# Performance work log

Measured on AMD Instinct MI355X. Metric: run time of the kernel, lower is better.

Reference implementation:

```python
import jax, jax.numpy as jnp
import numpy as np

T, H, N = 4096, 32, 64

def setup_inputs() -> dict:
    key = jax.random.key(0)
    ks = jax.random.split(key, 7)
    r = jax.random.normal(ks[0], (T, H, N), dtype=jnp.float32)
    w = jax.random.uniform(ks[1], (T, H, N), dtype=jnp.float32)  # decay in (0,1)
    k = jax.random.normal(ks[2], (T, H, N), dtype=jnp.float32)
    v = jax.random.normal(ks[3], (T, H, N), dtype=jnp.float32)
    a = jax.random.normal(ks[4], (T, H, N), dtype=jnp.float32) * 0.1
    b = jax.random.normal(ks[5], (T, H, N), dtype=jnp.float32) * 0.1
    state = jax.random.normal(ks[6], (H, N, N), dtype=jnp.float32) * 0.1
    return {"r": r, "w": w, "k": k, "v": v, "a": a, "b": b, "state": state}


def reference(r, w, k, v, a, b, state):
    # RWKV7 WKV recurrence (BlinkDL v7 reference):
    #   S_t = S_{t-1} * diag(w_t) + S_{t-1} @ (a_t b_t^T) + v_t k_t^T
    #   y_t = S_t @ r_t
    # state: [H, N, N] with rows = value dim, cols = key dim.
    def step(S, inp):
        r_, w_, k_, v_, a_, b_ = inp  # each [H, N]
        ab = jnp.einsum('hi,hj->hij', a_, b_)           # [H, N, N]
        vk = jnp.einsum('hi,hj->hij', v_, k_)           # [H, N, N]
        S = S * w_[:, None, :] + jnp.einsum('hij,hjk->hik', S, ab) + vk
        y = jnp.einsum('hij,hj->hi', S, r_)             # [H, N]
        return S, y

    S_final, y = jax.lax.scan(step, state, (r, w, k, v, a, b))
    return y, S_final  # y: [T, H, N], S_final: [H, N, N]
```

## Files before the change

### kernel.cpp

```cpp
#include <hip/hip_runtime.h>
#include <hip/hip_bf16.h>


#define Tt 4096
#define Hh 32
#define Nn 64
#define Ll 64
#define Cc 64
#define HN (Hh * Nn)
#define NN (Nn * Nn)

__device__ __forceinline__ float ldf(const float* p) { return *p; }
__device__ __forceinline__ float ldf(const __hip_bfloat16* p) { return __bfloat162float(*p); }
__device__ __forceinline__ void stf(float* p, float v) { *p = v; }
__device__ __forceinline__ void stf(__hip_bfloat16* p, float v) { *p = __float2bfloat16(v); }

__device__ __forceinline__ float rl(float v, int j) {
    return __int_as_float(__builtin_amdgcn_readlane(__float_as_int(v), j));
}

__device__ __forceinline__ float bflo(unsigned u) { return __uint_as_float(u << 16); }
__device__ __forceinline__ float bfhi(unsigned u) { return __uint_as_float(u & 0xffff0000u); }

template <typename ST>
__global__ __launch_bounds__(128, 4)
void pass1_scan(const float* __restrict__ rr, const float* __restrict__ ww,
                const float* __restrict__ kk, const float* __restrict__ vv,
                const float* __restrict__ aa, const float* __restrict__ bb,
                float* __restrict__ ylocal,
                ST* __restrict__ rho, ST* __restrict__ Mt, ST* __restrict__ Pt)
{
    const int c    = blockIdx.x >> 5;
    const int h    = blockIdx.x & 31;
    const int tid  = threadIdx.x;
    const int lane = tid & 63;
    const int wv   = tid >> 6;
    const int j0   = __builtin_amdgcn_readfirstlane(wv << 5);

    __shared__ float2 ex1[2][2][64];
    __shared__ float  ex2[2][2][64];

    float SP[32];
    float SM[32];
    #pragma unroll
    for (int jj = 0; jj < 32; ++jj) {
        SP[jj] = 0.0f;
        SM[jj] = (j0 + jj == lane) ? 1.0f : 0.0f;
    }

    int base = (c * Ll * Hh + h) * Nn;
    const int lv = j0 + (lane & 31);
    float ca = aa[base + lv];
    float cw = ww[base + lv];
    float cb = bb[base + lv];
    float cr = rr[base + lv];
    float ck = kk[base + lv];
    float cv = vv[base + lane];

    float py = 0.f, pq = 0.f;

    for (int t = 0; t < Ll; ++t) {
        float p0 = 0.f, p1 = 0.f, m0 = 0.f, m1 = 0.f;
        #pragma unroll
        for (int jj = 0; jj < 32; jj += 2) {
            const float a0 = rl(ca, jj), a1 = rl(ca, jj + 1);
            p0 += SP[jj + 0] * a0;  m0 += SM[jj + 0] * a0;
            p1 += SP[jj + 1] * a1;  m1 += SM[jj + 1] * a1;
        }
        const float pP = p0 + p1, pM = m0 + m1;

        ex1[t & 1][wv][lane] = make_float2(pP, pM);
        if (t > 0) ex2[(t - 1) & 1][wv][lane] = (wv == 0) ? pq : py;
        __syncthreads();
        const float2 o = ex1[t & 1][wv ^ 1][lane];
        const float saP = pP + o.x;
        const float saM = pM + o.y;
        if (t > 0) {
            const int ob = base - HN + lane;
            if (wv == 0) ylocal[ob] = py + ex2[(t - 1) & 1][1][lane];
            else         stf(&rho[ob], pq + ex2[(t - 1) & 1][0][lane]);
        }

        float na = 0.f, nw = 0.f, nb = 0.f, nr = 0.f, nk = 0.f, nv = 0.f;
        if (t + 1 < Ll) {
            const int b2 = base + HN;
            na = aa[b2 + lv]; nw = ww[b2 + lv]; nb = bb[b2 + lv];
            nr = rr[b2 + lv]; nk = kk[b2 + lv]; nv = vv[b2 + lane];
        }

        float y0 = 0.f, y1 = 0.f, q0 = 0.f, q1 = 0.f;
        #pragma unroll
        for (int jj = 0; jj < 32; jj += 2) {
            const float w0 = rl(cw, jj), w1 = rl(cw, jj + 1);
            const float b0 = rl(cb, jj), b1 = rl(cb, jj + 1);
            const float k0 = rl(ck, jj), k1 = rl(ck, jj + 1);
            const float r0 = rl(cr, jj), r1 = rl(cr, jj + 1);
            SP[jj + 0] = SP[jj + 0] * w0 + saP * b0 + cv * k0;
            SP[jj + 1] = SP[jj + 1] * w1 + saP * b1 + cv * k1;
            SM[jj + 0] = SM[jj + 0] * w0 + saM * b0;
            SM[jj + 1] = SM[jj + 1] * w1 + saM * b1;
            y0 += SP[jj + 0] * r0;
            y1 += SP[jj + 1] * r1;
            q0 += SM[jj + 0] * r0;
            q1 += SM[jj + 1] * r1;
        }
        py = y0 + y1;
        pq = q0 + q1;

        base += HN;
        ca = na; cw = nw; cb = nb; cr = nr; ck = nk; cv = nv;
    }

    {
        ex2[(Ll - 1) & 1][wv][lane] = (wv == 0) ? pq : py;
        __syncthreads();
        const int ob = base - HN + lane;
        if (wv == 0) ylocal[ob] = py + ex2[(Ll - 1) & 1][1][lane];
        else         stf(&rho[ob], pq + ex2[(Ll - 1) & 1][0][lane]);
    }

    const size_t mb = ((size_t)(c * Hh) + h) * NN;
    #pragma unroll
    for (int jj = 0; jj < 32; ++jj) {
        stf(&Pt[mb + (size_t)(j0 + jj) * Nn + lane], SP[jj]);
        stf(&Mt[mb + (size_t)(j0 + jj) * Nn + lane], SM[jj]);
    }
}

#define LMS 68

template <typename ST>
__global__ __launch_bounds__(512, 2)
void pass2_chain(const ST* __restrict__ Mt, const ST* __restrict__ Pt,
                 const float* __restrict__ st0, ST* __restrict__ Sst,
                 float* __restrict__ sfin)
{
    const int bid = blockIdx.x;
    const int h   = bid & 31;
    const int g   = bid >> 5;
    const int tid = threadIdx.x;
    const int j   = tid & 63;
    const int wv  = tid >> 6;
    const int r   = g * 8 + wv;

    __shared__ float lm[2][Nn][LMS];

    float s = st0[(h * Nn + r) * Nn + j];

    {
        const size_t mb = (size_t)h * NN;
        if constexpr (sizeof(ST) == 2) {
            const uint4 u = *(const uint4*)&Mt[mb + (size_t)tid * 8];
            const int jj = tid >> 3, kc = (tid & 7) * 8;
            float4 f0, f1;
            f0.x = bflo(u.x); f0.y = bfhi(u.x); f0.z = bflo(u.y); f0.w = bfhi(u.y);
            f1.x = bflo(u.z); f1.y = bfhi(u.z); f1.z = bflo(u.w); f1.w = bfhi(u.w);
            *(float4*)&lm[0][jj][kc]     = f0;
            *(float4*)&lm[0][jj][kc + 4] = f1;
        } else {
            const float4 q0 = *(const float4*)&Mt[mb + (size_t)tid * 4];
            const float4 q1 = *(const float4*)&Mt[mb + 2048 + (size_t)tid * 4];
            const int jj = tid >> 4, kc = (tid * 4) & 63;
            *(float4*)&lm[0][jj][kc]      = q0;
            *(float4*)&lm[0][32 + jj][kc] = q1;
        }
    }
    float pp = ldf(&Pt[(size_t)h * NN + (size_t)j * Nn + r]);
    __syncthreads();

    for (int c = 0; c < Cc; ++c) {
        const int buf = c & 1;
        stf(&Sst[((size_t)(c * Hh) + h) * NN + (size_t)r * Nn + j], s);

        const bool pf = (c + 1 < Cc);
        const size_t nb = ((size_t)((c + 1) * Hh) + h) * NN;
        uint4 u = {0, 0, 0, 0};
        float4 q0 = {0, 0, 0, 0}, q1 = {0, 0, 0, 0};
        float ppn = 0.f;
        if (pf) {
            if constexpr (sizeof(ST) == 2) {
                u = *(const uint4*)&Mt[nb + (size_t)tid * 8];
            } else {
                q0 = *(const float4*)&Mt[nb + (size_t)tid * 4];
                q1 = *(const float4*)&Mt[nb + 2048 + (size_t)tid * 4];
            }
            ppn = ldf(&Pt[nb + (size_t)j * Nn + r]);
        }

        float a0 = pp, a1 = 0.f, a2 = 0.f, a3 = 0.f;
        #pragma unroll
        for (int m = 0; m < 16; ++m) {
            const float4 mv = *(const float4*)&lm[buf][j][4 * m];
            a0 += rl(s, 4 * m + 0) * mv.x;
            a1 += rl(s, 4 * m + 1) * mv.y;
            a2 += rl(s, 4 * m + 2) * mv.z;
            a3 += rl(s, 4 * m + 3) * mv.w;
        }

        if (pf) {
            if constexpr (sizeof(ST) == 2) {
                const int jj = tid >> 3, kc = (tid & 7) * 8;
                float4 f0, f1;
                f0.x = bflo(u.x); f0.y = bfhi(u.x); f0.z = bflo(u.y); f0.w = bfhi(u.y);
                f1.x = bflo(u.z); f1.y = bfhi(u.z); f1.z = bflo(u.w); f1.w = bfhi(u.w);
                *(float4*)&lm[buf ^ 1][jj][kc]     = f0;
                *(float4*)&lm[buf ^ 1][jj][kc + 4] = f1;
            } else {
                const int jj = tid >> 4, kc = (tid * 4) & 63;
                *(float4*)&lm[buf ^ 1][jj][kc]      = q0;
                *(float4*)&lm[buf ^ 1][32 + jj][kc] = q1;
            }
        }

        s = (a0 + a1) + (a2 + a3);
        pp = ppn;
        __syncthreads();
    }

    sfin[(h * Nn + r) * Nn + j] = s;
}

template <typename ST>
__global__ __launch_bounds__(256, 4)
void pass3_fix(const ST* __restrict__ rho, const ST* __restrict__ Sst,
               float* __restrict__ y)
{
    const int c    = blockIdx.x >> 5;
    const int h    = blockIdx.x & 31;
    const int tid  = threadIdx.x;
    const int lane = tid & 63;
    const int tq   = tid >> 6;

    __shared__ float ls[Nn][LMS];

    const size_t sb = ((size_t)(c * Hh) + h) * NN;
    if constexpr (sizeof(ST) == 2) {
        #pragma unroll
        for (int half = 0; half < 2; ++half) {
            const int e = half * 2048 + tid * 8;
            const uint4 u = *(const uint4*)&Sst[sb + e];
            const int jj = e >> 6, kc = e & 63;
            float4 f0, f1;
            f0.x = bflo(u.x); f0.y = bfhi(u.x); f0.z = bflo(u.y); f0.w = bfhi(u.y);
            f1.x = bflo(u.z); f1.y = bfhi(u.z); f1.z = bflo(u.w); f1.w = bfhi(u.w);
            *(float4*)&ls[jj][kc]     = f0;
            *(float4*)&ls[jj][kc + 4] = f1;
        }
    } else {
        #pragma unroll
        for (int qq = 0; qq < 4; ++qq) {
            const int e = qq * 1024 + tid * 4;
            const float4 v = *(const float4*)&Sst[sb + e];
            *(float4*)&ls[e >> 6][e & 63] = v;
        }
    }

    float rt[16];
    #pragma unroll
    for (int m = 0; m < 16; ++m)
        rt[m] = ldf(&rho[((size_t)(c * Ll + tq * 16 + m) * Hh + h) * Nn + lane]);

    __syncthreads();

    float Srow[Nn];
    #pragma unroll
    for (int m = 0; m < 16; ++m) {
        const float4 v = *(const float4*)&ls[lane][4 * m];
        Srow[4*m+0] = v.x; Srow[4*m+1] = v.y; Srow[4*m+2] = v.z; Srow[4*m+3] = v.w;
    }

    #pragma unroll
    for (int m = 0; m < 16; ++m) {
        float a0 = 0.f, a1 = 0.f, a2 = 0.f, a3 = 0.f;
        #pragma unroll
        for (int j = 0; j < Nn; j += 4) {
            a0 += rl(rt[m], j + 0) * Srow[j + 0];
            a1 += rl(rt[m], j + 1) * Srow[j + 1];
            a2 += rl(rt[m], j + 2) * Srow[j + 2];
            a3 += rl(rt[m], j + 3) * Srow[j + 3];
        }
        const size_t oy = ((size_t)(c * Ll + tq * 16 + m) * Hh + h) * Nn + lane;
        y[oy] = y[oy] + ((a0 + a1) + (a2 + a3));
    }
}

__global__ __launch_bounds__(64, 1)
void seq_scan(const float* __restrict__ rr, const float* __restrict__ ww,
              const float* __restrict__ kk, const float* __restrict__ vv,
              const float* __restrict__ aa, const float* __restrict__ bb,
              const float* __restrict__ st0,
              float* __restrict__ y, float* __restrict__ sfin)
{
    const int h    = blockIdx.x;
    const int lane = threadIdx.x;

    float S[Nn];
    #pragma unroll
    for (int j = 0; j < Nn; ++j) S[j] = st0[(h * Nn + lane) * Nn + j];

    int base = h * Nn;
    float ca = aa[base + lane], cw = ww[base + lane], cb = bb[base + lane];
    float cr = rr[base + lane], ck = kk[base + lane], cv = vv[base + lane];

    for (int t = 0; t < Tt; ++t) {
        float na = 0.f, nw = 0.f, nb = 0.f, nr = 0.f, nk = 0.f, nv = 0.f;
        if (t + 1 < Tt) {
            const int b2 = base + HN + lane;
            na = aa[b2]; nw = ww[b2]; nb = bb[b2];
            nr = rr[b2]; nk = kk[b2]; nv = vv[b2];
        }

        float s0 = 0.f, s1 = 0.f;
        #pragma unroll
        for (int j = 0; j < Nn; j += 2) {
            s0 += S[j + 0] * rl(ca, j);
            s1 += S[j + 1] * rl(ca, j + 1);
        }
        const float sa = s0 + s1;

        float y0 = 0.f, y1 = 0.f;
        #pragma unroll
        for (int j = 0; j < Nn; j += 2) {
            const float w0 = rl(cw, j), w1 = rl(cw, j + 1);
            const float b0 = rl(cb, j), b1 = rl(cb, j + 1);
            const float k0 = rl(ck, j), k1 = rl(ck, j + 1);
            const float r0 = rl(cr, j), r1 = rl(cr, j + 1);
            S[j + 0] = S[j + 0] * w0 + sa * b0 + cv * k0;
            S[j + 1] = S[j + 1] * w1 + sa * b1 + cv * k1;
            y0 += S[j + 0] * r0;
            y1 += S[j + 1] * r1;
        }
        y[base + lane] = y0 + y1;
        base += HN;
        ca = na; cw = nw; cb = nb; cr = nr; ck = nk; cv = nv;
    }

    #pragma unroll
    for (int j = 0; j < Nn; ++j) sfin[(h * Nn + lane) * Nn + j] = S[j];
}

extern "C" void kernel_launch(void* const* d_in, const int* in_sizes, int n_in,
                              void* d_out, int out_size, void* d_ws, size_t ws_size,
                              hipStream_t stream)
{
    const float* r  = (const float*)d_in[0];
    const float* w  = (const float*)d_in[1];
    const float* k  = (const float*)d_in[2];
    const float* v  = (const float*)d_in[3];
    const float* a  = (const float*)d_in[4];
    const float* b  = (const float*)d_in[5];
    const float* st = (const float*)d_in[6];

    float* out  = (float*)d_out;
    float* yl   = out;
    float* sfin = out + (size_t)Tt * HN;

    const size_t nTHN = (size_t)Tt * HN;
    const size_t nCH  = (size_t)Cc * Hh * NN;
    const size_t need = nTHN + 3 * nCH;

    if (ws_size >= need * sizeof(float)) {
        float* ws  = (float*)d_ws;
        float* rho = ws;
        float* Mt  = ws + nTHN;
        float* Pt  = Mt + nCH;
        float* Ss  = Pt + nCH;
        hipLaunchKernelGGL((pass1_scan<float>), dim3(Cc * Hh), dim3(128), 0, stream,
                           r, w, k, v, a, b, yl, rho, Mt, Pt);
        hipLaunchKernelGGL((pass2_chain<float>), dim3(Hh * 8), dim3(512), 0, stream,
                           Mt, Pt, st, Ss, sfin);
        hipLaunchKernelGGL((pass3_fix<float>), dim3(Cc * Hh), dim3(256), 0, stream,
                           rho, Ss, out);
    } else if (ws_size >= need * sizeof(__hip_bfloat16)) {
        __hip_bfloat16* ws  = (__hip_bfloat16*)d_ws;
        __hip_bfloat16* rho = ws;
        __hip_bfloat16* Mt  = ws + nTHN;
        __hip_bfloat16* Pt  = Mt + nCH;
        __hip_bfloat16* Ss  = Pt + nCH;
        hipLaunchKernelGGL((pass1_scan<__hip_bfloat16>), dim3(Cc * Hh), dim3(128), 0, stream,
                           r, w, k, v, a, b, yl, rho, Mt, Pt);
        hipLaunchKernelGGL((pass2_chain<__hip_bfloat16>), dim3(Hh * 8), dim3(512), 0, stream,
                           Mt, Pt, st, Ss, sfin);
        hipLaunchKernelGGL((pass3_fix<__hip_bfloat16>), dim3(Cc * Hh), dim3(256), 0, stream,
                           rho, Ss, out);
    } else {
        hipLaunchKernelGGL(seq_scan, dim3(Hh), dim3(64), 0, stream,
                           r, w, k, v, a, b, st, yl, sfin);
    }
}
```

Before: 461.1 us.

## Split pass1 scan state across four waves and coalesce pass2 Pt loads via LDS

Pass1 now uses 256 threads per block, with each wave holding 16 state columns instead of 32. The partial dot products are reduced through shared memory across four waves, which halves the serial per-step work and register pressure per wave at the cost of more LDS traffic. Pass2 now loads the Pt correction term with a coalesced pattern into a small double-buffered LDS tile instead of doing strided per-thread global loads.

```diff
diff --git a/kernel.cpp b/kernel.cpp
--- a/kernel.cpp
+++ b/kernel.cpp
@@ -23,7 +23,7 @@
 __device__ __forceinline__ float bfhi(unsigned u) { return __uint_as_float(u & 0xffff0000u); }
 
 template <typename ST>
-__global__ __launch_bounds__(128, 4)
+__global__ __launch_bounds__(256, 8)
 void pass1_scan(const float* __restrict__ rr, const float* __restrict__ ww,
                 const float* __restrict__ kk, const float* __restrict__ vv,
                 const float* __restrict__ aa, const float* __restrict__ bb,
@@ -35,21 +35,22 @@
     const int tid  = threadIdx.x;
     const int lane = tid & 63;
     const int wv   = tid >> 6;
-    const int j0   = __builtin_amdgcn_readfirstlane(wv << 5);
-
-    __shared__ float2 ex1[2][2][64];
-    __shared__ float  ex2[2][2][64];
-
-    float SP[32];
-    float SM[32];
-    #pragma unroll
-    for (int jj = 0; jj < 32; ++jj) {
+    const int j0   = __builtin_amdgcn_readfirstlane(wv << 4);
+
+    __shared__ float2 ex1[2][4][64];
+    __shared__ float  exy[2][4][64];
+    __shared__ float  exq[2][4][64];
+
+    float SP[16];
+    float SM[16];
+    #pragma unroll
+    for (int jj = 0; jj < 16; ++jj) {
         SP[jj] = 0.0f;
         SM[jj] = (j0 + jj == lane) ? 1.0f : 0.0f;
     }
 
     int base = (c * Ll * Hh + h) * Nn;
-    const int lv = j0 + (lane & 31);
+    const int lv = j0 + (lane & 15);
     float ca = aa[base + lv];
     float cw = ww[base + lv];
     float cb = bb[base + lv];
@@ -62,7 +63,7 @@
     for (int t = 0; t < Ll; ++t) {
         float p0 = 0.f, p1 = 0.f, m0 = 0.f, m1 = 0.f;
         #pragma unroll
-        for (int jj = 0; jj < 32; jj += 2) {
+        for (int jj = 0; jj < 16; jj += 2) {
             const float a0 = rl(ca, jj), a1 = rl(ca, jj + 1);
             p0 += SP[jj + 0] * a0;  m0 += SM[jj + 0] * a0;
             p1 += SP[jj + 1] * a1;  m1 += SM[jj + 1] * a1;
@@ -70,15 +71,27 @@
         const float pP = p0 + p1, pM = m0 + m1;
 
         ex1[t & 1][wv][lane] = make_float2(pP, pM);
-        if (t > 0) ex2[(t - 1) & 1][wv][lane] = (wv == 0) ? pq : py;
+        if (t > 0) {
+            exy[(t - 1) & 1][wv][lane] = py;
+            exq[(t - 1) & 1][wv][lane] = pq;
+        }
         __syncthreads();
-        const float2 o = ex1[t & 1][wv ^ 1][lane];
-        const float saP = pP + o.x;
-        const float saM = pM + o.y;
+        const float2 e0 = ex1[t & 1][0][lane];
+        const float2 e1 = ex1[t & 1][1][lane];
+        const float2 e2 = ex1[t & 1][2][lane];
+        const float2 e3 = ex1[t & 1][3][lane];
+        const float saP = (e0.x + e1.x) + (e2.x + e3.x);
+        const float saM = (e0.y + e1.y) + (e2.y + e3.y);
         if (t > 0) {
+            const int p = (t - 1) & 1;
             const int ob = base - HN + lane;
-            if (wv == 0) ylocal[ob] = py + ex2[(t - 1) & 1][1][lane];
-            else         stf(&rho[ob], pq + ex2[(t - 1) & 1][0][lane]);
+            if (wv == 0) {
+                ylocal[ob] = (exy[p][0][lane] + exy[p][1][lane])
+                           + (exy[p][2][lane] + exy[p][3][lane]);
+            } else if (wv == 1) {
+                stf(&rho[ob], (exq[p][0][lane] + exq[p][1][lane])
+                            + (exq[p][2][lane] + exq[p][3][lane]));
+            }
         }
 
         float na = 0.f, nw = 0.f, nb = 0.f, nr = 0.f, nk = 0.f, nv = 0.f;
@@ -90,7 +103,7 @@
 
         float y0 = 0.f, y1 = 0.f, q0 = 0.f, q1 = 0.f;
         #pragma unroll
-        for (int jj = 0; jj < 32; jj += 2) {
+        for (int jj = 0; jj < 16; jj += 2) {
             const float w0 = rl(cw, jj), w1 = rl(cw, jj + 1);
             const float b0 = rl(cb, jj), b1 = rl(cb, jj + 1);
             const float k0 = rl(ck, jj), k1 = rl(ck, jj + 1);
@@ -112,16 +125,23 @@
     }
 
     {
-        ex2[(Ll - 1) & 1][wv][lane] = (wv == 0) ? pq : py;
+        const int p = (Ll - 1) & 1;
+        exy[p][wv][lane] = py;
+        exq[p][wv][lane] = pq;
         __syncthreads();
         const int ob = base - HN + lane;
-        if (wv == 0) ylocal[ob] = py + ex2[(Ll - 1) & 1][1][lane];
-        else         stf(&rho[ob], pq + ex2[(Ll - 1) & 1][0][lane]);
+        if (wv == 0) {
+            ylocal[ob] = (exy[p][0][lane] + exy[p][1][lane])
+                       + (exy[p][2][lane] + exy[p][3][lane]);
+        } else if (wv == 1) {
+            stf(&rho[ob], (exq[p][0][lane] + exq[p][1][lane])
+                        + (exq[p][2][lane] + exq[p][3][lane]));
+        }
     }
 
     const size_t mb = ((size_t)(c * Hh) + h) * NN;
     #pragma unroll
-    for (int jj = 0; jj < 32; ++jj) {
+    for (int jj = 0; jj < 16; ++jj) {
         stf(&Pt[mb + (size_t)(j0 + jj) * Nn + lane], SP[jj]);
         stf(&Mt[mb + (size_t)(j0 + jj) * Nn + lane], SM[jj]);
     }
@@ -144,8 +164,12 @@
     const int r   = g * 8 + wv;
 
     __shared__ float lm[2][Nn][LMS];
+    __shared__ float lpp[2][8][LMS];
 
     float s = st0[(h * Nn + r) * Nn + j];
+
+    const int pr = tid & 7, pc = tid >> 3;
+    const size_t poff = (size_t)pc * Nn + g * 8 + pr;
 
     {
         const size_t mb = (size_t)h * NN;
@@ -164,8 +188,8 @@
             *(float4*)&lm[0][jj][kc]      = q0;
             *(float4*)&lm[0][32 + jj][kc] = q1;
         }
-    }
-    float pp = ldf(&Pt[(size_t)h * NN + (size_t)j * Nn + r]);
+        lpp[0][pr][pc] = ldf(&Pt[mb + poff]);
+    }
     __syncthreads();
 
     for (int c = 0; c < Cc; ++c) {
@@ -176,7 +200,7 @@
         const size_t nb = ((size_t)((c + 1) * Hh) + h) * NN;
         uint4 u = {0, 0, 0, 0};
         float4 q0 = {0, 0, 0, 0}, q1 = {0, 0, 0, 0};
-        float ppn = 0.f;
+        float praw = 0.f;
         if (pf) {
             if constexpr (sizeof(ST) == 2) {
                 u = *(const uint4*)&Mt[nb + (size_t)tid * 8];
@@ -184,10 +208,10 @@
                 q0 = *(const float4*)&Mt[nb + (size_t)tid * 4];
                 q1 = *(const float4*)&Mt[nb + 2048 + (size_t)tid * 4];
             }
-            ppn = ldf(&Pt[nb + (size_t)j * Nn + r]);
-        }
-
-        float a0 = pp, a1 = 0.f, a2 = 0.f, a3 = 0.f;
+            praw = ldf(&Pt[nb + poff]);
+        }
+
+        float a0 = lpp[buf][wv][j], a1 = 0.f, a2 = 0.f, a3 = 0.f;
         #pragma unroll
         for (int m = 0; m < 16; ++m) {
             const float4 mv = *(const float4*)&lm[buf][j][4 * m];
@@ -210,10 +234,10 @@
                 *(float4*)&lm[buf ^ 1][jj][kc]      = q0;
                 *(float4*)&lm[buf ^ 1][32 + jj][kc] = q1;
             }
+            lpp[buf ^ 1][pr][pc] = praw;
         }
 
         s = (a0 + a1) + (a2 + a3);
-        pp = ppn;
         __syncthreads();
     }
 
@@ -365,7 +389,7 @@
         float* Mt  = ws + nTHN;
         float* Pt  = Mt + nCH;
         float* Ss  = Pt + nCH;
-        hipLaunchKernelGGL((pass1_scan<float>), dim3(Cc * Hh), dim3(128), 0, stream,
+        hipLaunchKernelGGL((pass1_scan<float>), dim3(Cc * Hh), dim3(256), 0, stream,
                            r, w, k, v, a, b, yl, rho, Mt, Pt);
         hipLaunchKernelGGL((pass2_chain<float>), dim3(Hh * 8), dim3(512), 0, stream,
                            Mt, Pt, st, Ss, sfin);
@@ -377,7 +401,7 @@
         __hip_bfloat16* Mt  = ws + nTHN;
         __hip_bfloat16* Pt  = Mt + nCH;
         __hip_bfloat16* Ss  = Pt + nCH;
-        hipLaunchKernelGGL((pass1_scan<__hip_bfloat16>), dim3(Cc * Hh), dim3(128), 0, stream,
+        hipLaunchKernelGGL((pass1_scan<__hip_bfloat16>), dim3(Cc * Hh), dim3(256), 0, stream,
                            r, w, k, v, a, b, yl, rho, Mt, Pt);
         hipLaunchKernelGGL((pass2_chain<__hip_bfloat16>), dim3(Hh * 8), dim3(512), 0, stream,
                            Mt, Pt, st, Ss, sfin);
```

After: 508.3 us. 10.2% more time.

## Pack P/M state into float2 vectors and split chain pass into smaller blocks

Applied to the files above, without the earlier changes.

Pass1 stores the P and M state columns as two-wide float vectors so the compiler can issue packed FMA instructions, and it exchanges y and q together through one shared buffer. Pass2 now runs 512 blocks of 256 threads instead of 256 blocks of 512, each block owning 4 state rows. Each block reloads the full M matrix per chunk, which doubles the redundant M traffic. The per-row P values are staged into shared memory through a coalesced load and then transposed.

```diff
diff --git a/kernel.cpp b/kernel.cpp
--- a/kernel.cpp
+++ b/kernel.cpp
@@ -9,6 +9,8 @@
 #define Cc 64
 #define HN (Hh * Nn)
 #define NN (Nn * Nn)
+
+typedef __attribute__((ext_vector_type(2))) float f32x2;
 
 __device__ __forceinline__ float ldf(const float* p) { return *p; }
 __device__ __forceinline__ float ldf(const __hip_bfloat16* p) { return __bfloat162float(*p); }
@@ -37,15 +39,14 @@
     const int wv   = tid >> 6;
     const int j0   = __builtin_amdgcn_readfirstlane(wv << 5);
 
-    __shared__ float2 ex1[2][2][64];
-    __shared__ float  ex2[2][2][64];
-
-    float SP[32];
-    float SM[32];
+    __shared__ f32x2 ex1[2][2][64];
+    __shared__ f32x2 exy[2][2][64];
+
+    f32x2 SPM[32];
     #pragma unroll
     for (int jj = 0; jj < 32; ++jj) {
-        SP[jj] = 0.0f;
-        SM[jj] = (j0 + jj == lane) ? 1.0f : 0.0f;
+        f32x2 ini; ini.x = 0.0f; ini.y = (j0 + jj == lane) ? 1.0f : 0.0f;
+        SPM[jj] = ini;
     }
 
     int base = (c * Ll * Hh + h) * Nn;
@@ -57,28 +58,28 @@
     float ck = kk[base + lv];
     float cv = vv[base + lane];
 
-    float py = 0.f, pq = 0.f;
+    f32x2 pyq = {0.f, 0.f};
 
     for (int t = 0; t < Ll; ++t) {
-        float p0 = 0.f, p1 = 0.f, m0 = 0.f, m1 = 0.f;
+        f32x2 pm0 = {0.f, 0.f}, pm1 = {0.f, 0.f};
         #pragma unroll
         for (int jj = 0; jj < 32; jj += 2) {
             const float a0 = rl(ca, jj), a1 = rl(ca, jj + 1);
-            p0 += SP[jj + 0] * a0;  m0 += SM[jj + 0] * a0;
-            p1 += SP[jj + 1] * a1;  m1 += SM[jj + 1] * a1;
-        }
-        const float pP = p0 + p1, pM = m0 + m1;
-
-        ex1[t & 1][wv][lane] = make_float2(pP, pM);
-        if (t > 0) ex2[(t - 1) & 1][wv][lane] = (wv == 0) ? pq : py;
+            pm0 += SPM[jj + 0] * a0;
+            pm1 += SPM[jj + 1] * a1;
+        }
+        const f32x2 pm = pm0 + pm1;
+
+        ex1[t & 1][wv][lane] = pm;
+        if (t > 0) exy[(t - 1) & 1][wv][lane] = pyq;
         __syncthreads();
-        const float2 o = ex1[t & 1][wv ^ 1][lane];
-        const float saP = pP + o.x;
-        const float saM = pM + o.y;
+        const f32x2 o  = ex1[t & 1][wv ^ 1][lane];
+        const f32x2 sa2 = pm + o;
         if (t > 0) {
+            const f32x2 oy = exy[(t - 1) & 1][wv ^ 1][lane];
             const int ob = base - HN + lane;
-            if (wv == 0) ylocal[ob] = py + ex2[(t - 1) & 1][1][lane];
-            else         stf(&rho[ob], pq + ex2[(t - 1) & 1][0][lane]);
+            if (wv == 0) ylocal[ob] = pyq.x + oy.x;
+            else         stf(&rho[ob], pyq.y + oy.y);
         }
 
         float na = 0.f, nw = 0.f, nb = 0.f, nr = 0.f, nk = 0.f, nv = 0.f;
@@ -88,49 +89,50 @@
             nr = rr[b2 + lv]; nk = kk[b2 + lv]; nv = vv[b2 + lane];
         }
 
-        float y0 = 0.f, y1 = 0.f, q0 = 0.f, q1 = 0.f;
+        f32x2 yq0 = {0.f, 0.f}, yq1 = {0.f, 0.f};
         #pragma unroll
         for (int jj = 0; jj < 32; jj += 2) {
             const float w0 = rl(cw, jj), w1 = rl(cw, jj + 1);
             const float b0 = rl(cb, jj), b1 = rl(cb, jj + 1);
             const float k0 = rl(ck, jj), k1 = rl(ck, jj + 1);
             const float r0 = rl(cr, jj), r1 = rl(cr, jj + 1);
-            SP[jj + 0] = SP[jj + 0] * w0 + saP * b0 + cv * k0;
-            SP[jj + 1] = SP[jj + 1] * w1 + saP * b1 + cv * k1;
-            SM[jj + 0] = SM[jj + 0] * w0 + saM * b0;
-            SM[jj + 1] = SM[jj + 1] * w1 + saM * b1;
-            y0 += SP[jj + 0] * r0;
-            y1 += SP[jj + 1] * r1;
-            q0 += SM[jj + 0] * r0;
-            q1 += SM[jj + 1] * r1;
-        }
-        py = y0 + y1;
-        pq = q0 + q1;
+            f32x2 t0 = SPM[jj + 0] * w0 + sa2 * b0;
+            f32x2 t1 = SPM[jj + 1] * w1 + sa2 * b1;
+            t0.x += cv * k0;
+            t1.x += cv * k1;
+            SPM[jj + 0] = t0;
+            SPM[jj + 1] = t1;
+            yq0 += t0 * r0;
+            yq1 += t1 * r1;
+        }
+        pyq = yq0 + yq1;
 
         base += HN;
         ca = na; cw = nw; cb = nb; cr = nr; ck = nk; cv = nv;
     }
 
     {
-        ex2[(Ll - 1) & 1][wv][lane] = (wv == 0) ? pq : py;
+        const int p = (Ll - 1) & 1;
+        exy[p][wv][lane] = pyq;
         __syncthreads();
+        const f32x2 oy = exy[p][wv ^ 1][lane];
         const int ob = base - HN + lane;
-        if (wv == 0) ylocal[ob] = py + ex2[(Ll - 1) & 1][1][lane];
-        else         stf(&rho[ob], pq + ex2[(Ll - 1) & 1][0][lane]);
+        if (wv == 0) ylocal[ob] = pyq.x + oy.x;
+        else         stf(&rho[ob], pyq.y + oy.y);
     }
 
     const size_t mb = ((size_t)(c * Hh) + h) * NN;
     #pragma unroll
     for (int jj = 0; jj < 32; ++jj) {
-        stf(&Pt[mb + (size_t)(j0 + jj) * Nn + lane], SP[jj]);
-        stf(&Mt[mb + (size_t)(j0 + jj) * Nn + lane], SM[jj]);
+        stf(&Pt[mb + (size_t)(j0 + jj) * Nn + lane], SPM[jj].x);
+        stf(&Mt[mb + (size_t)(j0 + jj) * Nn + lane], SPM[jj].y);
     }
 }
 
 #define LMS 68
 
 template <typename ST>
-__global__ __launch_bounds__(512, 2)
+__global__ __launch_bounds__(256, 4)
 void pass2_chain(const ST* __restrict__ Mt, const ST* __restrict__ Pt,
                  const float* __restrict__ st0, ST* __restrict__ Sst,
                  float* __restrict__ sfin)
@@ -141,31 +143,40 @@
     const int tid = threadIdx.x;
     const int j   = tid & 63;
     const int wv  = tid >> 6;
-    const int r   = g * 8 + wv;
+    const int r   = g * 4 + wv;
 
     __shared__ float lm[2][Nn][LMS];
+    __shared__ float lpp[2][4][LMS];
 
     float s = st0[(h * Nn + r) * Nn + j];
+
+    const int pr = tid & 3, pc = tid >> 2;
+    const size_t poff = (size_t)pc * Nn + g * 4 + pr;
 
     {
         const size_t mb = (size_t)h * NN;
         if constexpr (sizeof(ST) == 2) {
-            const uint4 u = *(const uint4*)&Mt[mb + (size_t)tid * 8];
-            const int jj = tid >> 3, kc = (tid & 7) * 8;
-            float4 f0, f1;
-            f0.x = bflo(u.x); f0.y = bfhi(u.x); f0.z = bflo(u.y); f0.w = bfhi(u.y);
-            f1.x = bflo(u.z); f1.y = bfhi(u.z); f1.z = bflo(u.w); f1.w = bfhi(u.w);
-            *(float4*)&lm[0][jj][kc]     = f0;
-            *(float4*)&lm[0][jj][kc + 4] = f1;
+            #pragma unroll
+            for (int half = 0; half < 2; ++half) {
+                const int e = half * 2048 + tid * 8;
+                const uint4 u = *(const uint4*)&Mt[mb + e];
+                const int jj = e >> 6, kc = e & 63;
+                float4 f0, f1;
+                f0.x = bflo(u.x); f0.y = bfhi(u.x); f0.z = bflo(u.y); f0.w = bfhi(u.y);
+                f1.x = bflo(u.z); f1.y = bfhi(u.z); f1.z = bflo(u.w); f1.w = bfhi(u.w);
+                *(float4*)&lm[0][jj][kc]     = f0;
+                *(float4*)&lm[0][jj][kc + 4] = f1;
+            }
         } else {
-            const float4 q0 = *(const float4*)&Mt[mb + (size_t)tid * 4];
-            const float4 q1 = *(const float4*)&Mt[mb + 2048 + (size_t)tid * 4];
-            const int jj = tid >> 4, kc = (tid * 4) & 63;
-            *(float4*)&lm[0][jj][kc]      = q0;
-            *(float4*)&lm[0][32 + jj][kc] = q1;
-        }
-    }
-    float pp = ldf(&Pt[(size_t)h * NN + (size_t)j * Nn + r]);
+            #pragma unroll
+            for (int qq = 0; qq < 4; ++qq) {
+                const int e = qq * 1024 + tid * 4;
+                const float4 q0 = *(const float4*)&Mt[mb + e];
+                *(float4*)&lm[0][e >> 6][e & 63] = q0;
+            }
+        }
+        lpp[0][pr][pc] = ldf(&Pt[mb + poff]);
+    }
     __syncthreads();
 
     for (int c = 0; c < Cc; ++c) {
@@ -174,20 +185,23 @@
 
         const bool pf = (c + 1 < Cc);
         const size_t nb = ((size_t)((c + 1) * Hh) + h) * NN;
-        uint4 u = {0, 0, 0, 0};
-        float4 q0 = {0, 0, 0, 0}, q1 = {0, 0, 0, 0};
-        float ppn = 0.f;
+        uint4 u0 = {0,0,0,0}, u1 = {0,0,0,0};
+        float4 q0 = {0,0,0,0}, q1 = {0,0,0,0}, q2 = {0,0,0,0}, q3 = {0,0,0,0};
+        float praw = 0.f;
         if (pf) {
             if constexpr (sizeof(ST) == 2) {
-                u = *(const uint4*)&Mt[nb + (size_t)tid * 8];
+                u0 = *(const uint4*)&Mt[nb + tid * 8];
+                u1 = *(const uint4*)&Mt[nb + 2048 + tid * 8];
             } else {
-                q0 = *(const float4*)&Mt[nb + (size_t)tid * 4];
-                q1 = *(const float4*)&Mt[nb + 2048 + (size_t)tid * 4];
+                q0 = *(const float4*)&Mt[nb + tid * 4];
+                q1 = *(const float4*)&Mt[nb + 1024 + tid * 4];
+                q2 = *(const float4*)&Mt[nb + 2048 + tid * 4];
+                q3 = *(const float4*)&Mt[nb + 3072 + tid * 4];
             }
-            ppn = ldf(&Pt[nb + (size_t)j * Nn + r]);
-        }
-
-        float a0 = pp, a1 = 0.f, a2 = 0.f, a3 = 0.f;
+            praw = ldf(&Pt[nb + poff]);
+        }
+
+        float a0 = lpp[buf][wv][j], a1 = 0.f, a2 = 0.f, a3 = 0.f;
         #pragma unroll
         for (int m = 0; m < 16; ++m) {
             const float4 mv = *(const float4*)&lm[buf][j][4 * m];
@@ -199,21 +213,36 @@
 
         if (pf) {
             if constexpr (sizeof(ST) == 2) {
-                const int jj = tid >> 3, kc = (tid & 7) * 8;
-                float4 f0, f1;
-                f0.x = bflo(u.x); f0.y = bfhi(u.x); f0.z = bflo(u.y); f0.w = bfhi(u.y);
-                f1.x = bflo(u.z); f1.y = bfhi(u.z); f1.z = bflo(u.w); f1.w = bfhi(u.w);
-                *(float4*)&lm[buf ^ 1][jj][kc]     = f0;
-                *(float4*)&lm[buf ^ 1][jj][kc + 4] = f1;
+                {
+                    const int e = tid * 8, jj = e >> 6, kc = e & 63;
+                    float4 f0, f1;
+                    f0.x = bflo(u0.x); f0.y = bfhi(u0.x); f0.z = bflo(u0.y); f0.w = bfhi(u0.y);
+                    f1.x = bflo(u0.z); f1.y = bfhi(u0.z); f1.z = bflo(u0.w); f1.w = bfhi(u0.w);
+                    *(float4*)&lm[buf ^ 1][jj][kc]     = f0;
+                    *(float4*)&lm[buf ^ 1][jj][kc + 4] = f1;
+                }
+                {
+                    const int e = 2048 + tid * 8, jj = e >> 6, kc = e & 63;
+                    float4 f0, f1;
+                    f0.x = bflo(u1.x); f0.y = bfhi(u1.x); f0.z = bflo(u1.y); f0.w = bfhi(u1.y);
+                    f1.x = bflo(u1.z); f1.y = bfhi(u1.z); f1.z = bflo(u1.w); f1.w = bfhi(u1.w);
+                    *(float4*)&lm[buf ^ 1][jj][kc]     = f0;
+                    *(float4*)&lm[buf ^ 1][jj][kc + 4] = f1;
+                }
             } else {
-                const int jj = tid >> 4, kc = (tid * 4) & 63;
-                *(float4*)&lm[buf ^ 1][jj][kc]      = q0;
-                *(float4*)&lm[buf ^ 1][32 + jj][kc] = q1;
+                const int e0 = tid * 4;
+                *(float4*)&lm[buf ^ 1][e0 >> 6][e0 & 63] = q0;
+                const int e1 = 1024 + tid * 4;
+                *(float4*)&lm[buf ^ 1][e1 >> 6][e1 & 63] = q1;
+                const int e2 = 2048 + tid * 4;
+                *(float4*)&lm[buf ^ 1][e2 >> 6][e2 & 63] = q2;
+                const int e3 = 3072 + tid * 4;
+                *(float4*)&lm[buf ^ 1][e3 >> 6][e3 & 63] = q3;
             }
+            lpp[buf ^ 1][pr][pc] = praw;
         }
 
         s = (a0 + a1) + (a2 + a3);
-        pp = ppn;
         __syncthreads();
     }
 
@@ -367,7 +396,7 @@
         float* Ss  = Pt + nCH;
         hipLaunchKernelGGL((pass1_scan<float>), dim3(Cc * Hh), dim3(128), 0, stream,
                            r, w, k, v, a, b, yl, rho, Mt, Pt);
-        hipLaunchKernelGGL((pass2_chain<float>), dim3(Hh * 8), dim3(512), 0, stream,
+        hipLaunchKernelGGL((pass2_chain<float>), dim3(Hh * 16), dim3(256), 0, stream,
                            Mt, Pt, st, Ss, sfin);
         hipLaunchKernelGGL((pass3_fix<float>), dim3(Cc * Hh), dim3(256), 0, stream,
                            rho, Ss, out);
@@ -379,7 +408,7 @@
         __hip_bfloat16* Ss  = Pt + nCH;
         hipLaunchKernelGGL((pass1_scan<__hip_bfloat16>), dim3(Cc * Hh), dim3(128), 0, stream,
                            r, w, k, v, a, b, yl, rho, Mt, Pt);
-        hipLaunchKernelGGL((pass2_chain<__hip_bfloat16>), dim3(Hh * 8), dim3(512), 0, stream,
+        hipLaunchKernelGGL((pass2_chain<__hip_bfloat16>), dim3(Hh * 16), dim3(256), 0, stream,
                            Mt, Pt, st, Ss, sfin);
         hipLaunchKernelGGL((pass3_fix<__hip_bfloat16>), dim3(Cc * Hh), dim3(256), 0, stream,
                            rho, Ss, out);
```

Measured after the change: 423.7 us. -8.1%, faster.
